# Kernel optimization log

Hardware: AMD Instinct MI355X
Metric: run time of the kernel (lower is better)

The kernel has to match this reference:

```python
import jax, jax.numpy as jnp
import numpy as np

FORCE = 8.0
N_STATE = 40
BATCH = 524288


def setup_inputs() -> dict:
    key = jax.random.key(0)
    x0 = jax.random.normal(key, (BATCH, N_STATE), dtype=jnp.float32)
    t = jnp.float32(0.0)          # unused: system is autonomous (torch code passes nan)
    dt = jnp.float32(0.05)        # canonical Lorenz96 RK4 step
    return {"x0": x0, "t": t, "dt": dt}


def _dxdt(x):
    # torch shift(x, n) == roll(x, -n, dims=-1)
    # dxdt = (shift(x,1) - shift(x,-2)) * shift(x,-1) - x + force
    return (jnp.roll(x, -1, axis=-1) - jnp.roll(x, 2, axis=-1)) * jnp.roll(x, 1, axis=-1) - x + FORCE


def reference(x0, t, dt):
    # Classic RK4 step (rk4_torch); t is ignored (autonomous RHS).
    k1 = _dxdt(x0)
    k2 = _dxdt(x0 + 0.5 * dt * k1)
    k3 = _dxdt(x0 + 0.5 * dt * k2)
    k4 = _dxdt(x0 + dt * k3)
    return x0 + (dt / 6.0) * (k1 + 2.0 * k2 + 2.0 * k3 + k4)
```

## Files before the change

kernel.cpp:

```cpp
#include <hip/hip_runtime.h>


#define FORCE 8.0f

__global__ __launch_bounds__(256)
void lorenz96_rk4_halo(const float4* __restrict__ x0,
                       const float* __restrict__ dt_p,
                       float4* __restrict__ out,
                       long nf4)
{
    const long tid  = (long)blockIdx.x * blockDim.x + threadIdx.x;
    const long wave = tid >> 6;
    const int  lane = (int)(tid & 63);
    const int  lrow = lane / 10;
    const int  c    = lane - lrow * 10;
    const long f    = wave * 60 + lane;
    if (lane >= 60 || f >= nf4) return;

    const long rowbase = wave * 60 + (long)lrow * 10;
    const int cm2 = (c >= 2) ? c - 2 : c + 8;
    const int cm1 = (c >= 1) ? c - 1 : c + 9;
    const int cp1 = (c <= 8) ? c + 1 : c - 9;

    const float4 vm2 = x0[rowbase + cm2];
    const float4 vm1 = x0[rowbase + cm1];
    const float4 v0  = x0[rowbase + c  ];
    const float4 vp1 = x0[rowbase + cp1];

    float xa[16];
    xa[0]=vm2.x; xa[1]=vm2.y; xa[2]=vm2.z; xa[3]=vm2.w;
    xa[4]=vm1.x; xa[5]=vm1.y; xa[6]=vm1.z; xa[7]=vm1.w;
    xa[8]=v0.x;  xa[9]=v0.y;  xa[10]=v0.z; xa[11]=v0.w;
    xa[12]=vp1.x; xa[13]=vp1.y; xa[14]=vp1.z; xa[15]=vp1.w;

    const float dt  = dt_p[0];
    const float hdt = 0.5f * dt;


    float k1[13], y1[13];
#pragma unroll
    for (int i = 0; i < 13; ++i)
        k1[i] = (xa[i+3] - xa[i]) * xa[i+1] - xa[i+2] + FORCE;
#pragma unroll
    for (int i = 0; i < 13; ++i)
        y1[i] = fmaf(hdt, k1[i], xa[i+2]);

    float k2[10], y2[10];
#pragma unroll
    for (int i = 0; i < 10; ++i)
        k2[i] = (y1[i+3] - y1[i]) * y1[i+1] - y1[i+2] + FORCE;
#pragma unroll
    for (int i = 0; i < 10; ++i)
        y2[i] = fmaf(hdt, k2[i], xa[i+4]);

    float k3[7], y3[7];
#pragma unroll
    for (int i = 0; i < 7; ++i)
        k3[i] = (y2[i+3] - y2[i]) * y2[i+1] - y2[i+2] + FORCE;
#pragma unroll
    for (int i = 0; i < 7; ++i)
        y3[i] = fmaf(dt, k3[i], xa[i+6]);

    float k4[4];
#pragma unroll
    for (int i = 0; i < 4; ++i)
        k4[i] = (y3[i+3] - y3[i]) * y3[i+1] - y3[i+2] + FORCE;

    const float sc = dt * (1.0f / 6.0f);
    float acc[4];
#pragma unroll
    for (int m = 0; m < 4; ++m) {
        float t = k1[m+6] + k4[m];
        t = fmaf(2.0f, k2[m+4], t);
        t = fmaf(2.0f, k3[m+2], t);
        acc[m] = t;
    }
    float4 r;
    r.x = fmaf(sc, acc[0], xa[8]);
    r.y = fmaf(sc, acc[1], xa[9]);
    r.z = fmaf(sc, acc[2], xa[10]);
    r.w = fmaf(sc, acc[3], xa[11]);
    out[f] = r;
}

extern "C" void kernel_launch(void* const* d_in, const int* in_sizes, int n_in,
                              void* d_out, int out_size, void* d_ws, size_t ws_size,
                              hipStream_t stream) {
    const float4* x0 = (const float4*)d_in[0];
    const float* dt = (const float*)d_in[2];
    float4* out = (float4*)d_out;

    const long nf4 = (long)in_sizes[0] / 4;
    const long nwaves = (nf4 + 59) / 60;
    const int block = 256;
    const long grid = (nwaves + 3) / 4;
    lorenz96_rk4_halo<<<dim3((unsigned)grid), dim3(block), 0, stream>>>(x0, dt, out, nf4);
}
```

Baseline: 149.1 us.

## Process four float4 chunks per thread with staggered loads and full lane use

Each thread now handles four float4 outputs spaced 64 apart, computing row and column indices per element instead of mapping 60 of 64 lanes to 6 rows. Loads for later chunks are issued before earlier chunks are computed, so memory latency overlaps with arithmetic. Index math moves to 32-bit unsigned. This removes the 4 idle lanes per wave and cuts the grid fourfold, at the cost of more registers per thread and a division by 10 per chunk.

```diff
diff --git a/kernel.cpp b/kernel.cpp
--- a/kernel.cpp
+++ b/kernel.cpp
@@ -3,39 +3,15 @@
 
 #define FORCE 8.0f
 
-__global__ __launch_bounds__(256)
-void lorenz96_rk4_halo(const float4* __restrict__ x0,
-                       const float* __restrict__ dt_p,
-                       float4* __restrict__ out,
-                       long nf4)
+__device__ __forceinline__ float4 rk4_chunk(const float4 vm2, const float4 vm1,
+                                            const float4 v0,  const float4 vp1,
+                                            const float dt,   const float hdt)
 {
-    const long tid  = (long)blockIdx.x * blockDim.x + threadIdx.x;
-    const long wave = tid >> 6;
-    const int  lane = (int)(tid & 63);
-    const int  lrow = lane / 10;
-    const int  c    = lane - lrow * 10;
-    const long f    = wave * 60 + lane;
-    if (lane >= 60 || f >= nf4) return;
-
-    const long rowbase = wave * 60 + (long)lrow * 10;
-    const int cm2 = (c >= 2) ? c - 2 : c + 8;
-    const int cm1 = (c >= 1) ? c - 1 : c + 9;
-    const int cp1 = (c <= 8) ? c + 1 : c - 9;
-
-    const float4 vm2 = x0[rowbase + cm2];
-    const float4 vm1 = x0[rowbase + cm1];
-    const float4 v0  = x0[rowbase + c  ];
-    const float4 vp1 = x0[rowbase + cp1];
-
     float xa[16];
-    xa[0]=vm2.x; xa[1]=vm2.y; xa[2]=vm2.z; xa[3]=vm2.w;
-    xa[4]=vm1.x; xa[5]=vm1.y; xa[6]=vm1.z; xa[7]=vm1.w;
-    xa[8]=v0.x;  xa[9]=v0.y;  xa[10]=v0.z; xa[11]=v0.w;
+    xa[0]=vm2.x;  xa[1]=vm2.y;  xa[2]=vm2.z;  xa[3]=vm2.w;
+    xa[4]=vm1.x;  xa[5]=vm1.y;  xa[6]=vm1.z;  xa[7]=vm1.w;
+    xa[8]=v0.x;   xa[9]=v0.y;   xa[10]=v0.z;  xa[11]=v0.w;
     xa[12]=vp1.x; xa[13]=vp1.y; xa[14]=vp1.z; xa[15]=vp1.w;
-
-    const float dt  = dt_p[0];
-    const float hdt = 0.5f * dt;
-
 
     float k1[13], y1[13];
 #pragma unroll
@@ -67,20 +43,73 @@
         k4[i] = (y3[i+3] - y3[i]) * y3[i+1] - y3[i+2] + FORCE;
 
     const float sc = dt * (1.0f / 6.0f);
-    float acc[4];
-#pragma unroll
-    for (int m = 0; m < 4; ++m) {
-        float t = k1[m+6] + k4[m];
-        t = fmaf(2.0f, k2[m+4], t);
-        t = fmaf(2.0f, k3[m+2], t);
-        acc[m] = t;
+    float4 r;
+    {
+        float t0 = k1[6] + k4[0]; t0 = fmaf(2.0f, k2[4], t0); t0 = fmaf(2.0f, k3[2], t0);
+        float t1 = k1[7] + k4[1]; t1 = fmaf(2.0f, k2[5], t1); t1 = fmaf(2.0f, k3[3], t1);
+        float t2 = k1[8] + k4[2]; t2 = fmaf(2.0f, k2[6], t2); t2 = fmaf(2.0f, k3[4], t2);
+        float t3 = k1[9] + k4[3]; t3 = fmaf(2.0f, k2[7], t3); t3 = fmaf(2.0f, k3[5], t3);
+        r.x = fmaf(sc, t0, xa[8]);
+        r.y = fmaf(sc, t1, xa[9]);
+        r.z = fmaf(sc, t2, xa[10]);
+        r.w = fmaf(sc, t3, xa[11]);
     }
-    float4 r;
-    r.x = fmaf(sc, acc[0], xa[8]);
-    r.y = fmaf(sc, acc[1], xa[9]);
-    r.z = fmaf(sc, acc[2], xa[10]);
-    r.w = fmaf(sc, acc[3], xa[11]);
-    out[f] = r;
+    return r;
+}
+
+__global__ __launch_bounds__(256)
+void lorenz96_rk4_halo4(const float4* __restrict__ x0,
+                        const float* __restrict__ dt_p,
+                        float4* __restrict__ out,
+                        unsigned nf4)
+{
+    const unsigned tid  = blockIdx.x * blockDim.x + threadIdx.x;
+    const unsigned w    = tid >> 6;
+    const unsigned lane = tid & 63u;
+    const unsigned fb   = w * 256u + lane;
+
+    const float dt  = dt_p[0];
+    const float hdt = 0.5f * dt;
+
+    float4 a0_, a1_, a2_, a3_;
+    float4 b0_, b1_, b2_, b3_;
+    float4 c0_, c1_, c2_, c3_;
+    float4 d0_, d1_, d2_, d3_;
+    unsigned f0_, f1_, f2_, f3_;
+    bool act0, act1, act2, act3;
+
+#define LOADC(J, A, B, C, D, F, ACT)                                         \
+    {                                                                        \
+        F = fb + 64u * (J);                                                  \
+        ACT = (F < nf4);                                                     \
+        if (ACT) {                                                           \
+            const unsigned r  = F / 10u;                                     \
+            const unsigned c  = F - r * 10u;                                 \
+            const unsigned rb = r * 10u;                                     \
+            const unsigned cm2 = (c >= 2u) ? c - 2u : c + 8u;                \
+            const unsigned cm1 = (c >= 1u) ? c - 1u : c + 9u;                \
+            const unsigned cp1 = (c <= 8u) ? c + 1u : c - 9u;                \
+            A = x0[rb + cm2];                                                \
+            B = x0[rb + cm1];                                                \
+            C = x0[rb + c  ];                                                \
+            D = x0[rb + cp1];                                                \
+        }                                                                    \
+    }
+
+#define COMPC(A, B, C, D, F, ACT)                                            \
+    if (ACT) { out[F] = rk4_chunk(A, B, C, D, dt, hdt); }
+
+    LOADC(0, a0_, b0_, c0_, d0_, f0_, act0)
+    LOADC(1, a1_, b1_, c1_, d1_, f1_, act1)
+    LOADC(2, a2_, b2_, c2_, d2_, f2_, act2)
+    COMPC(a0_, b0_, c0_, d0_, f0_, act0)
+    LOADC(3, a3_, b3_, c3_, d3_, f3_, act3)
+    COMPC(a1_, b1_, c1_, d1_, f1_, act1)
+    COMPC(a2_, b2_, c2_, d2_, f2_, act2)
+    COMPC(a3_, b3_, c3_, d3_, f3_, act3)
+
+#undef LOADC
+#undef COMPC
 }
 
 extern "C" void kernel_launch(void* const* d_in, const int* in_sizes, int n_in,
@@ -90,9 +119,9 @@
     const float* dt = (const float*)d_in[2];
     float4* out = (float4*)d_out;
 
-    const long nf4 = (long)in_sizes[0] / 4;
-    const long nwaves = (nf4 + 59) / 60;
+    const unsigned nf4 = (unsigned)((long)in_sizes[0] / 4);
+    const unsigned nwaves = (nf4 + 255u) / 256u;
     const int block = 256;
-    const long grid = (nwaves + 3) / 4;
-    lorenz96_rk4_halo<<<dim3((unsigned)grid), dim3(block), 0, stream>>>(x0, dt, out, nf4);
+    const unsigned grid = (nwaves + 3u) / 4u;
+    lorenz96_rk4_halo4<<<dim3(grid), dim3(block), 0, stream>>>(x0, dt, out, nf4);
 }
```

New measurement: 151.2 us. About the same (+1.4%).

## Share row halos through LDS with 320-thread blocks and nontemporal stores

Applied to the files above, without the earlier changes.

The new main kernel has each thread load only its own float4 into shared memory and read its three neighbours from LDS, where the old kernel issued four global loads per thread and left 4 of every 64 lanes idle. The block size of 320 matches 32 rows of 10 float4s, so every lane does useful work. Output is written with nontemporal stores, and the RHS is rewritten as a single fma per term. The LDS path adds a block barrier and only applies when the element count divides by 320; other sizes fall back to a simplified halo kernel.

```diff
diff --git a/kernel.cpp b/kernel.cpp
--- a/kernel.cpp
+++ b/kernel.cpp
@@ -2,6 +2,96 @@
 
 
 #define FORCE 8.0f
+
+typedef float f32x4 __attribute__((ext_vector_type(4)));
+
+__device__ __forceinline__ void nt_store(float4* p, const float4& v) {
+    __builtin_nontemporal_store(*(const f32x4*)&v, (f32x4*)p);
+}
+
+__device__ __forceinline__ float4 rk4_chunk(const float4 vm2, const float4 vm1,
+                                            const float4 v0,  const float4 vp1,
+                                            const float dt,   const float hdt)
+{
+    float xa[16];
+    xa[0]=vm2.x;  xa[1]=vm2.y;  xa[2]=vm2.z;  xa[3]=vm2.w;
+    xa[4]=vm1.x;  xa[5]=vm1.y;  xa[6]=vm1.z;  xa[7]=vm1.w;
+    xa[8]=v0.x;   xa[9]=v0.y;   xa[10]=v0.z;  xa[11]=v0.w;
+    xa[12]=vp1.x; xa[13]=vp1.y; xa[14]=vp1.z; xa[15]=vp1.w;
+
+    float k1[13], y1[13];
+#pragma unroll
+    for (int i = 0; i < 13; ++i)
+        k1[i] = fmaf(xa[i+3] - xa[i], xa[i+1], FORCE - xa[i+2]);
+#pragma unroll
+    for (int i = 0; i < 13; ++i)
+        y1[i] = fmaf(hdt, k1[i], xa[i+2]);
+
+    float k2[10], y2[10];
+#pragma unroll
+    for (int i = 0; i < 10; ++i)
+        k2[i] = fmaf(y1[i+3] - y1[i], y1[i+1], FORCE - y1[i+2]);
+#pragma unroll
+    for (int i = 0; i < 10; ++i)
+        y2[i] = fmaf(hdt, k2[i], xa[i+4]);
+
+    float k3[7], y3[7];
+#pragma unroll
+    for (int i = 0; i < 7; ++i)
+        k3[i] = fmaf(y2[i+3] - y2[i], y2[i+1], FORCE - y2[i+2]);
+#pragma unroll
+    for (int i = 0; i < 7; ++i)
+        y3[i] = fmaf(dt, k3[i], xa[i+6]);
+
+    float k4[4];
+#pragma unroll
+    for (int i = 0; i < 4; ++i)
+        k4[i] = fmaf(y3[i+3] - y3[i], y3[i+1], FORCE - y3[i+2]);
+
+    const float sc = dt * (1.0f / 6.0f);
+    float4 r;
+    float t0 = k1[6] + k4[0]; t0 = fmaf(2.0f, k2[4], t0); t0 = fmaf(2.0f, k3[2], t0);
+    float t1 = k1[7] + k4[1]; t1 = fmaf(2.0f, k2[5], t1); t1 = fmaf(2.0f, k3[3], t1);
+    float t2 = k1[8] + k4[2]; t2 = fmaf(2.0f, k2[6], t2); t2 = fmaf(2.0f, k3[4], t2);
+    float t3 = k1[9] + k4[3]; t3 = fmaf(2.0f, k2[7], t3); t3 = fmaf(2.0f, k3[5], t3);
+    r.x = fmaf(sc, t0, xa[8]);
+    r.y = fmaf(sc, t1, xa[9]);
+    r.z = fmaf(sc, t2, xa[10]);
+    r.w = fmaf(sc, t3, xa[11]);
+    return r;
+}
+
+__global__ __launch_bounds__(320)
+void lorenz96_rk4_lds(const float4* __restrict__ x0,
+                      const float* __restrict__ dt_p,
+                      float4* __restrict__ out)
+{
+    __shared__ float4 tile[320];
+
+    const unsigned tid = threadIdx.x;
+    const unsigned f   = blockIdx.x * 320u + tid;
+
+    const float4 own = x0[f];
+    tile[tid] = own;
+
+    const float dt  = dt_p[0];
+    const float hdt = 0.5f * dt;
+
+    const unsigned c   = tid % 10u;
+    const unsigned rb  = tid - c;
+    const unsigned im2 = rb + ((c >= 2u) ? c - 2u : c + 8u);
+    const unsigned im1 = rb + ((c >= 1u) ? c - 1u : c + 9u);
+    const unsigned ip1 = rb + ((c <= 8u) ? c + 1u : c - 9u);
+
+    __syncthreads();
+
+    const float4 vm2 = tile[im2];
+    const float4 vm1 = tile[im1];
+    const float4 vp1 = tile[ip1];
+
+    const float4 r = rk4_chunk(vm2, vm1, own, vp1, dt, hdt);
+    nt_store(&out[f], r);
+}
 
 __global__ __launch_bounds__(256)
 void lorenz96_rk4_halo(const float4* __restrict__ x0,
@@ -9,78 +99,24 @@
                        float4* __restrict__ out,
                        long nf4)
 {
-    const long tid  = (long)blockIdx.x * blockDim.x + threadIdx.x;
-    const long wave = tid >> 6;
-    const int  lane = (int)(tid & 63);
-    const int  lrow = lane / 10;
-    const int  c    = lane - lrow * 10;
-    const long f    = wave * 60 + lane;
-    if (lane >= 60 || f >= nf4) return;
-
-    const long rowbase = wave * 60 + (long)lrow * 10;
+    const long f = (long)blockIdx.x * blockDim.x + threadIdx.x;
+    if (f >= nf4) return;
+    const long r  = f / 10;
+    const int  c  = (int)(f - r * 10);
+    const long rb = r * 10;
     const int cm2 = (c >= 2) ? c - 2 : c + 8;
     const int cm1 = (c >= 1) ? c - 1 : c + 9;
     const int cp1 = (c <= 8) ? c + 1 : c - 9;
 
-    const float4 vm2 = x0[rowbase + cm2];
-    const float4 vm1 = x0[rowbase + cm1];
-    const float4 v0  = x0[rowbase + c  ];
-    const float4 vp1 = x0[rowbase + cp1];
-
-    float xa[16];
-    xa[0]=vm2.x; xa[1]=vm2.y; xa[2]=vm2.z; xa[3]=vm2.w;
-    xa[4]=vm1.x; xa[5]=vm1.y; xa[6]=vm1.z; xa[7]=vm1.w;
-    xa[8]=v0.x;  xa[9]=v0.y;  xa[10]=v0.z; xa[11]=v0.w;
-    xa[12]=vp1.x; xa[13]=vp1.y; xa[14]=vp1.z; xa[15]=vp1.w;
+    const float4 vm2 = x0[rb + cm2];
+    const float4 vm1 = x0[rb + cm1];
+    const float4 v0  = x0[rb + c  ];
+    const float4 vp1 = x0[rb + cp1];
 
     const float dt  = dt_p[0];
     const float hdt = 0.5f * dt;
-
-
-    float k1[13], y1[13];
-#pragma unroll
-    for (int i = 0; i < 13; ++i)
-        k1[i] = (xa[i+3] - xa[i]) * xa[i+1] - xa[i+2] + FORCE;
-#pragma unroll
-    for (int i = 0; i < 13; ++i)
-        y1[i] = fmaf(hdt, k1[i], xa[i+2]);
-
-    float k2[10], y2[10];
-#pragma unroll
-    for (int i = 0; i < 10; ++i)
-        k2[i] = (y1[i+3] - y1[i]) * y1[i+1] - y1[i+2] + FORCE;
-#pragma unroll
-    for (int i = 0; i < 10; ++i)
-        y2[i] = fmaf(hdt, k2[i], xa[i+4]);
-
-    float k3[7], y3[7];
-#pragma unroll
-    for (int i = 0; i < 7; ++i)
-        k3[i] = (y2[i+3] - y2[i]) * y2[i+1] - y2[i+2] + FORCE;
-#pragma unroll
-    for (int i = 0; i < 7; ++i)
-        y3[i] = fmaf(dt, k3[i], xa[i+6]);
-
-    float k4[4];
-#pragma unroll
-    for (int i = 0; i < 4; ++i)
-        k4[i] = (y3[i+3] - y3[i]) * y3[i+1] - y3[i+2] + FORCE;
-
-    const float sc = dt * (1.0f / 6.0f);
-    float acc[4];
-#pragma unroll
-    for (int m = 0; m < 4; ++m) {
-        float t = k1[m+6] + k4[m];
-        t = fmaf(2.0f, k2[m+4], t);
-        t = fmaf(2.0f, k3[m+2], t);
-        acc[m] = t;
-    }
-    float4 r;
-    r.x = fmaf(sc, acc[0], xa[8]);
-    r.y = fmaf(sc, acc[1], xa[9]);
-    r.z = fmaf(sc, acc[2], xa[10]);
-    r.w = fmaf(sc, acc[3], xa[11]);
-    out[f] = r;
+    const float4 res = rk4_chunk(vm2, vm1, v0, vp1, dt, hdt);
+    nt_store(&out[f], res);
 }
 
 extern "C" void kernel_launch(void* const* d_in, const int* in_sizes, int n_in,
@@ -91,8 +127,14 @@
     float4* out = (float4*)d_out;
 
     const long nf4 = (long)in_sizes[0] / 4;
-    const long nwaves = (nf4 + 59) / 60;
-    const int block = 256;
-    const long grid = (nwaves + 3) / 4;
-    lorenz96_rk4_halo<<<dim3((unsigned)grid), dim3(block), 0, stream>>>(x0, dt, out, nf4);
+
+    if (nf4 % 320 == 0) {
+        const unsigned grid = (unsigned)(nf4 / 320);
+        lorenz96_rk4_lds<<<dim3(grid), dim3(320), 0, stream>>>(x0, dt, out);
+    } else {
+        const int block = 256;
+        const long grid = (nf4 + block - 1) / block;
+        lorenz96_rk4_halo<<<dim3((unsigned)grid), dim3(block), 0, stream>>>(
+            x0, dt, out, nf4);
+    }
 }
```

After: 147.2 us. About the same (-1.3%).
